# Performance work log

Measured on AMD Instinct MI355X. Metric: run time of the kernel, lower is better.

## Reference

```python
import jax, jax.numpy as jnp
import numpy as np

# dims
F, V, E, NIN, NOUT = 4, 4, 64, 1024, 1024
M = NIN + 2
# args constants
GMIN, GMAX, EPS, PGMIN = 0.01, 1.0, 0.1, 0.1
ETA2 = 0.25          # ACT[0].eta_fault[0,2]
ACT_T, NEG_T = 1.0, 1.0

# stand-in printed-electronics nonlinearities (ACT list and INV list)
_ACT = [lambda z: jax.nn.sigmoid(4.0 * (z - 0.5)), lambda z: jnp.tanh(z)]
_INV = [lambda a: 1.0 - a, lambda a: jax.nn.sigmoid(4.0 * (0.5 - a))]


def setup_inputs() -> dict:
    key = jax.random.key(0)
    ks = jax.random.split(key, 8)
    a = jax.random.uniform(ks[0], (F, V, E, NIN), jnp.float32)
    theta = jax.random.uniform(ks[1], (M, NOUT), jnp.float32) / 100.0 + GMIN
    theta = theta.at[-1, :].add(GMAX)
    theta = theta.at[-2, :].set(ETA2 / (1.0 - ETA2) * (theta[:-2, :].sum(0) + theta[-1, :]))
    coeff_act = jax.random.uniform(ks[2], (2, NOUT), jnp.float32, minval=-0.5, maxval=0.5)
    coeff_neg = jax.random.uniform(ks[3], (2, M), jnp.float32, minval=-0.5, maxval=0.5)
    noise_u = jax.random.uniform(ks[4], (F, V, M, NOUT), jnp.float32)
    gum = lambda k, s: -jnp.log(-jnp.log(jax.random.uniform(k, s, jnp.float32) + 1e-20) + 1e-20)
    gum_act = gum(ks[5], (2, NOUT))
    gum_neg = gum(ks[6], (2, M))
    fault_mask = jnp.ones((F, M, NOUT), jnp.float32)
    return dict(a=a, theta_=theta, coeff_act=coeff_act, coeff_neg=coeff_neg,
                noise_u=noise_u, gum_act=gum_act, gum_neg=gum_neg, fault_mask=fault_mask)


def _st_clip(x, lo, hi):
    sg = jax.lax.stop_gradient
    return x + sg(jnp.clip(x, lo, hi) - x)


def _gumbel_st(c, g, temp):
    # clamp, gumbel-softmax, hard argmax with straight-through estimator
    sg = jax.lax.stop_gradient
    cc = _st_clip(c, -1.0, 1.0)
    alpha = jax.nn.softmax((cc + g) / temp, axis=0)
    hard = jax.nn.one_hot(jnp.argmax(alpha, 0), c.shape[0], axis=0, dtype=alpha.dtype)
    return sg(hard) + alpha - sg(alpha)


def _forward(a, theta_, coeff_act, coeff_neg, noise_u, gum_act, gum_neg, fault_mask):
    sg = jax.lax.stop_gradient
    # theta property: clamp, zero small magnitudes (straight-through)
    tc = _st_clip(theta_, -GMAX, GMAX)
    tz = jnp.where(jnp.abs(tc) < GMIN, 0.0, tc)
    theta = sg(tz) + tc - sg(tc)
    # theta_noisy [F,V,M,N]: repeat + multiplicative uniform noise + fault mask
    tn = theta[None, None] * ((noise_u * 2.0 - 1.0) * EPS + 1.0) * fault_mask[:, None]
    at = jnp.abs(tn)
    W = at / (at.sum(axis=2, keepdims=True) + 1e-10)
    pos = (tn >= 0).astype(W.dtype)
    neg = 1.0 - pos
    # a_extend [F,V,E,M]: append bias-one and zero columns
    ones = jnp.ones(a.shape[:3] + (1,), a.dtype)
    ax = jnp.concatenate([a, ones, jnp.zeros_like(ones)], axis=-1)
    beta = _gumbel_st(coeff_neg, gum_neg, NEG_T)      # [2,M]
    an = beta[0] * _INV[0](ax) + beta[1] * _INV[1](ax)
    an = an.at[..., -1].set(0.0)
    z = (jnp.einsum('fvem,fvmn->fven', ax, W * pos)
         + jnp.einsum('fvem,fvmn->fven', an, W * neg))
    # MAC_power: vectorized expansion of sum_{f,v,m,n} g[m,n]*||sel - y||^2 over e
    gi = jnp.abs(tc)
    gt = gi * (PGMIN / gi.min(axis=0, keepdims=True))  # g_tilde [M,N]
    p = sg(pos)
    q = 1.0 - p
    AA = jnp.einsum('fvem,fvem->fvm', ax, ax)
    BB = jnp.einsum('fvem,fvem->fvm', an, an)
    AY = jnp.einsum('fvem,fven->fvmn', ax, z)
    BY = jnp.einsum('fvem,fven->fvmn', an, z)
    YY = jnp.einsum('fven,fven->fvn', z, z)
    power = (jnp.einsum('mn,fvmn,fvm->', gt, p, AA)
             + jnp.einsum('mn,fvmn,fvm->', gt, q, BB)
             - 2.0 * (jnp.einsum('mn,fvmn,fvmn->', gt, p, AY)
                      + jnp.einsum('mn,fvmn,fvmn->', gt, q, BY))
             + jnp.einsum('n,fvn->', gt.sum(0), YY)) / (E * V * F)
    # Gumbel-mixed activation
    alpha = _gumbel_st(coeff_act, gum_act, ACT_T)      # [2,N]
    a_new = alpha[0] * _ACT[0](z) + alpha[1] * _ACT[1](z)
    return a_new, power


def reference(a, theta_, coeff_act, coeff_neg, noise_u, gum_act, gum_neg, fault_mask):
    return _forward(a, theta_, coeff_act, coeff_neg, noise_u, gum_act, gum_neg, fault_mask)
```

## Files before the change

### kernel.cpp

```cpp
#include <hip/hip_runtime.h>

typedef float f32x4 __attribute__((ext_vector_type(4)));
typedef short bf16x8 __attribute__((ext_vector_type(8)));

#define NE 64
#define ND 1024
#define MM 1026

#define WS_GMINP 1050624
#define WS_GABSP 1083392
#define WS_AA    1642504
#define WS_BB    1658888
#define WS_TFG   1675272
#define WS_AXB   5877768
#define WS_ANB   6402056
#define POWER_IDX 1048576

__device__ __forceinline__ float frcp(float x) { return __builtin_amdgcn_rcpf(x); }
__device__ __forceinline__ unsigned f2b(float x) {
  unsigned u = __float_as_uint(x);
  u += 0x7FFF + ((u >> 16) & 1);
  return u >> 16;
}
__device__ __forceinline__ float b2f(unsigned b) { return __uint_as_float(b << 16); }
__device__ __forceinline__ float clamp1(float x) { return fminf(fmaxf(x, -1.f), 1.f); }

__global__ __launch_bounds__(256) void k_pre(
    const float* __restrict__ a, const float* __restrict__ theta_,
    const float* __restrict__ fault, const float* __restrict__ coeff_neg,
    const float* __restrict__ gum_neg, float* __restrict__ ws,
    float* __restrict__ out) {
  int bid = blockIdx.x, t = threadIdx.x;
  __shared__ float la[256][8];
  __shared__ float lb[256][8];
  __shared__ float beta_l[32];

  if (bid < 512) {
    int f = bid >> 7, chunk = bid & 127;
    int m0 = chunk * 8, m1 = (chunk == 127) ? MM : m0 + 8;
    unsigned* tfg = (unsigned*)(ws + WS_TFG) + (size_t)f * MM * ND;
    const float* fslab = fault + (size_t)f * MM * ND;
    int n4 = t * 4;
    for (int m = m0; m < m1; m++) {
      float4 tv = *(const float4*)(theta_ + m * ND + n4);
      float4 fl = *(const float4*)(fslab + (size_t)m * ND + n4);
      float c0 = clamp1(tv.x), c1 = clamp1(tv.y), c2 = clamp1(tv.z), c3 = clamp1(tv.w);
      float z0 = fabsf(c0), z1 = fabsf(c1), z2 = fabsf(c2), z3 = fabsf(c3);
      float w0 = (z0 < 0.01f ? 0.f : c0) * fl.x;
      float w1 = (z1 < 0.01f ? 0.f : c1) * fl.y;
      float w2 = (z2 < 0.01f ? 0.f : c2) * fl.z;
      float w3 = (z3 < 0.01f ? 0.f : c3) * fl.w;
      uint4 o;
      o.x = (f2b(z0) << 16) | f2b(w0);
      o.y = (f2b(z1) << 16) | f2b(w1);
      o.z = (f2b(z2) << 16) | f2b(w2);
      o.w = (f2b(z3) << 16) | f2b(w3);
      *(uint4*)(tfg + (size_t)m * ND + n4) = o;
    }
  } else if (bid < 1024) {
    int bb = bid - 512;
    int kc = bb & 31, fv = bb >> 5;
    if (t < 32) {
      int m = kc * 32 + t;
      float c0 = clamp1(coeff_neg[m]);
      float c1 = clamp1(coeff_neg[MM + m]);
      beta_l[t] = ((c1 + gum_neg[MM + m]) > (c0 + gum_neg[m])) ? 1.f : 0.f;
    }
    __syncthreads();
    int em = t >> 6, l = t & 63;
    int e = em * 16 + (l & 15);
    int g = (l >> 4) & 3;
    int kk = kc * 32 + g * 4;
    const float* ap = a + ((size_t)fv * NE + e) * 1024;
    float4 x0 = *(const float4*)(ap + kk);
    float4 x1 = *(const float4*)(ap + kk + 16);
    float xs[8] = {x0.x, x0.y, x0.z, x0.w, x1.x, x1.y, x1.z, x1.w};
    unsigned axp[8], anp[8];
#pragma unroll
    for (int j = 0; j < 8; j++) {
      int mloc = g * 4 + ((j < 4) ? j : 12 + j);
      float x = xs[j];
      float bs = beta_l[mloc];
      float an = (bs != 0.f) ? frcp(1.f + __expf(fmaf(4.f, x, -2.f))) : (1.f - x);
      axp[j] = f2b(x);
      anp[j] = f2b(an);
      la[t][j] = x * x;
      lb[t][j] = an * an;
    }
    uint4 ox = {axp[0] | (axp[1] << 16), axp[2] | (axp[3] << 16),
                axp[4] | (axp[5] << 16), axp[6] | (axp[7] << 16)};
    uint4 on = {anp[0] | (anp[1] << 16), anp[2] | (anp[3] << 16),
                anp[4] | (anp[5] << 16), anp[6] | (anp[7] << 16)};
    size_t bidx = ((size_t)(fv * 32 + kc) * 4 + em) * 64 + l;
    ((uint4*)(ws + WS_AXB))[bidx] = ox;
    ((uint4*)(ws + WS_ANB))[bidx] = on;
    __syncthreads();
    if (t < 32) {
      int g2 = (t >> 2) & 3, j2 = (t & 3) + 4 * (t >> 4);
      float sa = 0.f, sb = 0.f;
#pragma unroll
      for (int em2 = 0; em2 < 4; em2++)
#pragma unroll
        for (int i = 0; i < 16; i++) {
          sa += la[em2 * 64 + g2 * 16 + i][j2];
          sb += lb[em2 * 64 + g2 * 16 + i][j2];
        }
      ws[WS_AA + fv * 1024 + kc * 32 + t] = sa;
      ws[WS_BB + fv * 1024 + kc * 32 + t] = sb;
    }
  } else {
    int r = bid - 1024;
    int ng = r & 3, chunk = r >> 2;
    int n = ng * 256 + t;
    int m0 = chunk * 32, m1 = (chunk == 31) ? MM : m0 + 32;
    float mn = 1e30f, sm = 0.f;
    for (int m = m0; m < m1; m++) {
      float g = fabsf(clamp1(theta_[m * ND + n]));
      mn = fminf(mn, g);
      sm += g;
    }
    ws[WS_GMINP + chunk * ND + n] = mn;
    ws[WS_GABSP + chunk * ND + n] = sm;
    if (r == 0 && t == 0) out[POWER_IDX] = 0.f;
  }
}

union U8 { uint4 u; bf16x8 h; };

#define SLOAD(S, MC)                                                       \
  {                                                                        \
    _Pragma("unroll") for (int r = 0; r < 4; r++) {                        \
      size_t row = (size_t)((MC) + mb + r) * ND;                           \
      uA##S[r] = nslab[row + n0 + nin];                                    \
      uB##S[r] = nslab[row + n0 + 16 + nin];                               \
      tgA##S[r] = tslab[row + n0 + nin];                                   \
      tgB##S[r] = tslab[row + n0 + 16 + nin];                              \
    }                                                                      \
  }

#define AABBLOAD(MC)                                                       \
  {                                                                        \
    aa0 = *(const float4*)(AAp + (MC) + mb);                               \
    bb0 = *(const float4*)(BBp + (MC) + mb);                               \
  }

#define SWRITE(P, S)                                                       \
  {                                                                        \
    float aas[4] = {aa0.x, aa0.y, aa0.z, aa0.w};                           \
    float bbs[4] = {bb0.x, bb0.y, bb0.z, bb0.w};                           \
    unsigned wpu[2][4], wnu[2][4], gpu[2][4], gqu[2][4];                   \
    _Pragma("unroll") for (int h = 0; h < 2; h++) {                        \
      _Pragma("unroll") for (int r = 0; r < 4; r++) {                      \
        unsigned tg = h ? tgB##S[r] : tgA##S[r];                           \
        float u = h ? uB##S[r] : uA##S[r];                                 \
        unsigned neg = (tg >> 15) & 1;                                     \
        float aw = b2f(tg & 0x7FFF) * fmaf(u, 0.2f, 0.9f);                 \
        if (h) sacc1 += aw; else sacc0 += aw;                              \
        unsigned wb = f2b(aw);                                             \
        unsigned gb = tg >> 16;                                            \
        wpu[h][r] = neg ? 0u : wb;  wnu[h][r] = neg ? wb : 0u;             \
        gpu[h][r] = neg ? 0u : gb;  gqu[h][r] = neg ? gb : 0u;             \
        float tca = b2f(gb);                                               \
        float t1c = tca * (neg ? bbs[r] : aas[r]);                         \
        if (h) pacc1b += t1c; else pacc1a += t1c;                          \
      }                                                                    \
    }                                                                      \
    _Pragma("unroll") for (int pn = 0; pn < 4; pn++) {                     \
      uint2* pp = (uint2*)&panels[P][pn][0];                               \
      _Pragma("unroll") for (int h = 0; h < 2; h++) {                      \
        const unsigned* v = pn == 0 ? wpu[h] : pn == 1 ? wnu[h]            \
                             : pn == 2 ? gpu[h] : gqu[h];                  \
        int s0i = ((c_s * 2 + h) * 64 + (g0 & 3) * 16 + nin) * 2 + j0q;    \
        pp[s0i] = make_uint2(v[0] | (v[1] << 16), v[2] | (v[3] << 16));    \
      }                                                                    \
    }                                                                      \
  }

#define ALOAD(KS)                                                          \
  {                                                                        \
    _Pragma("unroll") for (int c = 0; c < 2; c++)                          \
      _Pragma("unroll") for (int mi = 0; mi < 2; mi++) {                   \
        size_t bi = ((size_t)(fv * 32 + (KS) * 2 + c) * 4 + eh * 2 + mi) * 64 + l; \
        axr[c][mi] = axbp[bi];                                             \
        anr[c][mi] = anbp[bi];                                             \
      }                                                                    \
  }

#define BMFMA(P)                                                           \
  {                                                                        \
    _Pragma("unroll") for (int c = 0; c < 2; c++) {                        \
      int bslot = (c * 2 + wn) * 64 + l;                                   \
      U8 bwp, bwn, bgp, bgq;                                               \
      bwp.u = panels[P][0][bslot]; bwn.u = panels[P][1][bslot];            \
      bgp.u = panels[P][2][bslot]; bgq.u = panels[P][3][bslot];            \
      _Pragma("unroll") for (int mi = 0; mi < 2; mi++) {                   \
        U8 ax, an; ax.u = axr[c][mi]; an.u = anr[c][mi];                   \
        accz[mi] = __builtin_amdgcn_mfma_f32_16x16x32_bf16(ax.h, bwp.h, accz[mi], 0, 0, 0); \
        accz[mi] = __builtin_amdgcn_mfma_f32_16x16x32_bf16(an.h, bwn.h, accz[mi], 0, 0, 0); \
        accg[mi] = __builtin_amdgcn_mfma_f32_16x16x32_bf16(ax.h, bgp.h, accg[mi], 0, 0, 0); \
        accg[mi] = __builtin_amdgcn_mfma_f32_16x16x32_bf16(an.h, bgq.h, accg[mi], 0, 0, 0); \
      }                                                                    \
    }                                                                      \
  }

#define BAR() __syncthreads()

__global__ __launch_bounds__(256) void k_main(
    const float* __restrict__ noise, const float* __restrict__ ws_c,
    const float* __restrict__ coeff_act, const float* __restrict__ gum_act,
    const float* __restrict__ coeff_neg, const float* __restrict__ gum_neg,
    float* __restrict__ out) {
  const int tid = threadIdx.x;
  const int w4 = tid >> 6, l = tid & 63;
  const int wn = w4 & 1;
  const int eh = w4 >> 1;
  const int fv = blockIdx.y, f = fv >> 2;
  const int n0 = blockIdx.x * 32;

  __shared__ uint4 panels[2][4][256];
  __shared__ float smin_l[32], gabs_l[32], s_l[32], gsum_l[32];

  if (tid < 32) {
    float mn = 1e30f;
#pragma unroll 8
    for (int c = 0; c < 32; c++) mn = fminf(mn, ws_c[WS_GMINP + c * ND + n0 + tid]);
    smin_l[tid] = mn;
  } else if (tid < 64) {
    int n = tid - 32;
    float s = 0.f;
#pragma unroll 8
    for (int c = 0; c < 32; c++) s += ws_c[WS_GABSP + c * ND + n0 + n];
    gabs_l[n] = s;
  }
  __syncthreads();
  if (tid < 32) {
    float s = 0.1f * frcp(smin_l[tid]);
    s_l[tid] = s;
    gsum_l[tid] = s * gabs_l[tid];
  }

  const int nin = tid & 15;
  const int mb = (tid >> 4) * 4;
  const int c_s = mb >> 5;
  const int g0 = (mb & 31) >> 2;
  const int j0q = (mb & 31) >> 4;
  const unsigned* tslab = (const unsigned*)(ws_c + WS_TFG) + (size_t)f * MM * ND;
  const float* nslab = noise + (size_t)fv * MM * ND;
  const float* AAp = ws_c + WS_AA + fv * 1024;
  const float* BBp = ws_c + WS_BB + fv * 1024;
  const uint4* axbp = (const uint4*)(ws_c + WS_AXB);
  const uint4* anbp = (const uint4*)(ws_c + WS_ANB);

  float pacc = 0.f, pacc1a = 0.f, pacc1b = 0.f, sacc0 = 0.f, sacc1 = 0.f;
  float uA0[4], uB0[4], uA1[4], uB1[4];
  unsigned tgA0[4], tgB0[4], tgA1[4], tgB1[4];
  float4 aa0, bb0;
  uint4 axr[2][2], anr[2][2];
  f32x4 accz[2] = {};
  f32x4 accg[2] = {};

  AABBLOAD(0);
  SLOAD(0, 0);
  SWRITE(0, 0);
  SLOAD(1, 64);
  BAR();

  for (int ks2 = 0; ks2 < 16; ks2 += 2) {
    ALOAD(ks2);
    AABBLOAD((ks2 + 1) * 64);
    if (ks2 < 14) SLOAD(0, (ks2 + 2) * 64);
    SWRITE(1, 1);
    BMFMA(0);
    BAR();
    ALOAD(ks2 + 1);
    if (ks2 < 14) {
      AABBLOAD((ks2 + 2) * 64);
      SLOAD(1, (ks2 + 3) * 64);
      SWRITE(0, 0);
    }
    BMFMA(1);
    BAR();
  }

  float* lds_f = (float*)&panels[0][0][0];
  lds_f[(tid >> 4) * 32 + nin] = sacc0;
  lds_f[(tid >> 4) * 32 + 16 + nin] = sacc1;
  __syncthreads();

  const int n_loc = wn * 16 + (l & 15);
  const int n_e = n0 + n_loc;
  float S = 0.f;
#pragma unroll
  for (int mg = 0; mg < 16; mg++) S += lds_f[mg * 32 + n_loc];

  const float s_ne = s_l[n_loc];
  unsigned tg24 = tslab[(size_t)1024 * ND + n_e];
  unsigned tg25 = tslab[(size_t)1025 * ND + n_e];
  float u24 = nslab[(size_t)1024 * ND + n_e];
  float u25 = nslab[(size_t)1025 * ND + n_e];
  float w24 = b2f(tg24 & 0x7FFF) * fmaf(u24, 0.2f, 0.9f);
  float w25 = b2f(tg25 & 0x7FFF) * fmaf(u25, 0.2f, 0.9f);
  S += w24 + w25;
  const float invS = frcp(S + 1e-10f);

  float cn0 = clamp1(coeff_neg[1024]), cn1 = clamp1(coeff_neg[MM + 1024]);
  const float anb = ((cn1 + gum_neg[MM + 1024]) > (cn0 + gum_neg[1024]))
                        ? frcp(1.f + __expf(2.f)) : 0.f;
  float ca0 = clamp1(coeff_act[n_e]), ca1 = clamp1(coeff_act[ND + n_e]);
  const float alv = ((ca1 + gum_act[ND + n_e]) > (ca0 + gum_act[n_e])) ? 1.f : 0.f;

  unsigned neg24 = (tg24 >> 15) & 1;
  float sel24 = neg24 ? anb : 1.f;
  float ztail = w24 * invS * sel24;
  float gt24 = b2f(tg24 >> 16) * s_ne;
  if (l < 16 && eh == 0) pacc += 64.f * gt24 * sel24 * sel24;

  const float gsn = gsum_l[n_loc];
  float zsum = 0.f;
#pragma unroll
  for (int mi = 0; mi < 2; mi++) {
#pragma unroll
    for (int r = 0; r < 4; r++) {
      float z = accz[mi][r] * invS + ztail;
      zsum += z;
      pacc += gsn * z * z - 2.f * z * (accg[mi][r] * s_ne);
      float s0v = frcp(1.f + __expf(fmaf(-4.f, z, 2.f)));
      float t1v = 1.f - 2.f * frcp(__expf(2.f * z) + 1.f);
      int e = (eh * 2 + mi) * 16 + ((l >> 4) & 3) * 4 + r;
      out[((size_t)(fv * NE + e)) * ND + n_e] = (alv != 0.f) ? t1v : s0v;
    }
  }
  pacc -= 2.f * zsum * (gt24 * sel24);
  pacc += s_l[nin] * pacc1a + s_l[16 + nin] * pacc1b;

  float* red = lds_f + 1024;
  red[tid] = pacc;
  __syncthreads();
  for (int s = 128; s > 0; s >>= 1) {
    if (tid < s) red[tid] += red[tid + s];
    __syncthreads();
  }
  if (tid == 0) atomicAdd(out + POWER_IDX, red[0] * (1.f / 1024.f));
}

extern "C" void kernel_launch(void* const* d_in, const int* in_sizes, int n_in,
                              void* d_out, int out_size, void* d_ws, size_t ws_size,
                              hipStream_t stream) {
  const float* a = (const float*)d_in[0];
  const float* theta_ = (const float*)d_in[1];
  const float* coeff_act = (const float*)d_in[2];
  const float* coeff_neg = (const float*)d_in[3];
  const float* noise_u = (const float*)d_in[4];
  const float* gum_act = (const float*)d_in[5];
  const float* gum_neg = (const float*)d_in[6];
  const float* fault = (const float*)d_in[7];
  float* out = (float*)d_out;
  float* ws = (float*)d_ws;

  k_pre<<<1152, 256, 0, stream>>>(a, theta_, fault, coeff_neg, gum_neg, ws, out);
  k_main<<<dim3(32, 16), 256, 0, stream>>>(noise_u, ws, coeff_act, gum_act,
                                           coeff_neg, gum_neg, out);
}
```

Measured before the change: 174.3 us.

## Fold per-column theta min/sum reduction into main kernel's streaming loop

Removes the separate k_pre branch that reduced |theta| per column into partial min/sum buffers, and instead computes column min and sum inside k_main from the bf16 |theta| values it already streams, reducing them through LDS at the end. The theta-packing work in k_pre is split into more, smaller blocks, with the two tail rows handled by four extra blocks. Noise loads are marked nontemporal. The intent is to drop a pass over theta and the prologue reductions in k_main, at the cost of using bf16-rounded |theta| for the min/sum and extra LDS traffic.

After: 163.2 us. 1.07x faster.

```diff
diff --git a/kernel.cpp b/kernel.cpp
--- a/kernel.cpp
+++ b/kernel.cpp
@@ -7,8 +7,6 @@
 #define ND 1024
 #define MM 1026
 
-#define WS_GMINP 1050624
-#define WS_GABSP 1083392
 #define WS_AA    1642504
 #define WS_BB    1658888
 #define WS_TFG   1675272
@@ -35,13 +33,15 @@
   __shared__ float lb[256][8];
   __shared__ float beta_l[32];
 
-  if (bid < 512) {
-    int f = bid >> 7, chunk = bid & 127;
-    int m0 = chunk * 8, m1 = (chunk == 127) ? MM : m0 + 8;
+  if (bid < 1024) {
+    int f = bid >> 8, chunk = bid & 255;
+    int m0 = chunk * 4;
     unsigned* tfg = (unsigned*)(ws + WS_TFG) + (size_t)f * MM * ND;
     const float* fslab = fault + (size_t)f * MM * ND;
     int n4 = t * 4;
-    for (int m = m0; m < m1; m++) {
+#pragma unroll
+    for (int r = 0; r < 4; r++) {
+      int m = m0 + r;
       float4 tv = *(const float4*)(theta_ + m * ND + n4);
       float4 fl = *(const float4*)(fslab + (size_t)m * ND + n4);
       float c0 = clamp1(tv.x), c1 = clamp1(tv.y), c2 = clamp1(tv.z), c3 = clamp1(tv.w);
@@ -57,8 +57,9 @@
       o.w = (f2b(z3) << 16) | f2b(w3);
       *(uint4*)(tfg + (size_t)m * ND + n4) = o;
     }
-  } else if (bid < 1024) {
-    int bb = bid - 512;
+    if (bid == 0 && t == 0) out[POWER_IDX] = 0.f;
+  } else if (bid < 1536) {
+    int bb = bid - 1024;
     int kc = bb & 31, fv = bb >> 5;
     if (t < 32) {
       int m = kc * 32 + t;
@@ -109,19 +110,28 @@
       ws[WS_BB + fv * 1024 + kc * 32 + t] = sb;
     }
   } else {
-    int r = bid - 1024;
-    int ng = r & 3, chunk = r >> 2;
-    int n = ng * 256 + t;
-    int m0 = chunk * 32, m1 = (chunk == 31) ? MM : m0 + 32;
-    float mn = 1e30f, sm = 0.f;
-    for (int m = m0; m < m1; m++) {
-      float g = fabsf(clamp1(theta_[m * ND + n]));
-      mn = fminf(mn, g);
-      sm += g;
-    }
-    ws[WS_GMINP + chunk * ND + n] = mn;
-    ws[WS_GABSP + chunk * ND + n] = sm;
-    if (r == 0 && t == 0) out[POWER_IDX] = 0.f;
+    int f = bid - 1536;
+    unsigned* tfg = (unsigned*)(ws + WS_TFG) + (size_t)f * MM * ND;
+    const float* fslab = fault + (size_t)f * MM * ND;
+    int n4 = t * 4;
+#pragma unroll
+    for (int r = 0; r < 2; r++) {
+      int m = 1024 + r;
+      float4 tv = *(const float4*)(theta_ + m * ND + n4);
+      float4 fl = *(const float4*)(fslab + (size_t)m * ND + n4);
+      float c0 = clamp1(tv.x), c1 = clamp1(tv.y), c2 = clamp1(tv.z), c3 = clamp1(tv.w);
+      float z0 = fabsf(c0), z1 = fabsf(c1), z2 = fabsf(c2), z3 = fabsf(c3);
+      float w0 = (z0 < 0.01f ? 0.f : c0) * fl.x;
+      float w1 = (z1 < 0.01f ? 0.f : c1) * fl.y;
+      float w2 = (z2 < 0.01f ? 0.f : c2) * fl.z;
+      float w3 = (z3 < 0.01f ? 0.f : c3) * fl.w;
+      uint4 o;
+      o.x = (f2b(z0) << 16) | f2b(w0);
+      o.y = (f2b(z1) << 16) | f2b(w1);
+      o.z = (f2b(z2) << 16) | f2b(w2);
+      o.w = (f2b(z3) << 16) | f2b(w3);
+      *(uint4*)(tfg + (size_t)m * ND + n4) = o;
+    }
   }
 }
 
@@ -131,8 +141,8 @@
   {                                                                        \
     _Pragma("unroll") for (int r = 0; r < 4; r++) {                        \
       size_t row = (size_t)((MC) + mb + r) * ND;                           \
-      uA##S[r] = nslab[row + n0 + nin];                                    \
-      uB##S[r] = nslab[row + n0 + 16 + nin];                               \
+      uA##S[r] = __builtin_nontemporal_load(nslab + row + n0 + nin);       \
+      uB##S[r] = __builtin_nontemporal_load(nslab + row + n0 + 16 + nin);  \
       tgA##S[r] = tslab[row + n0 + nin];                                   \
       tgB##S[r] = tslab[row + n0 + 16 + nin];                              \
     }                                                                      \
@@ -162,7 +172,8 @@
         gpu[h][r] = neg ? 0u : gb;  gqu[h][r] = neg ? gb : 0u;             \
         float tca = b2f(gb);                                               \
         float t1c = tca * (neg ? bbs[r] : aas[r]);                         \
-        if (h) pacc1b += t1c; else pacc1a += t1c;                          \
+        if (h) { pacc1b += t1c; mnacc1 = fminf(mnacc1, tca); gsacc1 += tca; } \
+        else   { pacc1a += t1c; mnacc0 = fminf(mnacc0, tca); gsacc0 += tca; } \
       }                                                                    \
     }                                                                      \
     _Pragma("unroll") for (int pn = 0; pn < 4; pn++) {                     \
@@ -218,26 +229,6 @@
   const int n0 = blockIdx.x * 32;
 
   __shared__ uint4 panels[2][4][256];
-  __shared__ float smin_l[32], gabs_l[32], s_l[32], gsum_l[32];
-
-  if (tid < 32) {
-    float mn = 1e30f;
-#pragma unroll 8
-    for (int c = 0; c < 32; c++) mn = fminf(mn, ws_c[WS_GMINP + c * ND + n0 + tid]);
-    smin_l[tid] = mn;
-  } else if (tid < 64) {
-    int n = tid - 32;
-    float s = 0.f;
-#pragma unroll 8
-    for (int c = 0; c < 32; c++) s += ws_c[WS_GABSP + c * ND + n0 + n];
-    gabs_l[n] = s;
-  }
-  __syncthreads();
-  if (tid < 32) {
-    float s = 0.1f * frcp(smin_l[tid]);
-    s_l[tid] = s;
-    gsum_l[tid] = s * gabs_l[tid];
-  }
 
   const int nin = tid & 15;
   const int mb = (tid >> 4) * 4;
@@ -252,6 +243,7 @@
   const uint4* anbp = (const uint4*)(ws_c + WS_ANB);
 
   float pacc = 0.f, pacc1a = 0.f, pacc1b = 0.f, sacc0 = 0.f, sacc1 = 0.f;
+  float mnacc0 = 1e30f, mnacc1 = 1e30f, gsacc0 = 0.f, gsacc1 = 0.f;
   float uA0[4], uB0[4], uA1[4], uB1[4];
   unsigned tgA0[4], tgB0[4], tgA1[4], tgB1[4];
   float4 aa0, bb0;
@@ -283,17 +275,23 @@
   }
 
   float* lds_f = (float*)&panels[0][0][0];
-  lds_f[(tid >> 4) * 32 + nin] = sacc0;
-  lds_f[(tid >> 4) * 32 + 16 + nin] = sacc1;
+  const int gi_ = (tid >> 4) * 32;
+  lds_f[gi_ + nin] = sacc0;           lds_f[gi_ + 16 + nin] = sacc1;
+  lds_f[512 + gi_ + nin] = mnacc0;    lds_f[512 + gi_ + 16 + nin] = mnacc1;
+  lds_f[1024 + gi_ + nin] = gsacc0;   lds_f[1024 + gi_ + 16 + nin] = gsacc1;
+  lds_f[1536 + gi_ + nin] = pacc1a;   lds_f[1536 + gi_ + 16 + nin] = pacc1b;
   __syncthreads();
 
   const int n_loc = wn * 16 + (l & 15);
   const int n_e = n0 + n_loc;
-  float S = 0.f;
-#pragma unroll
-  for (int mg = 0; mg < 16; mg++) S += lds_f[mg * 32 + n_loc];
-
-  const float s_ne = s_l[n_loc];
+  float S = 0.f, MN = 1e30f, GS = 0.f;
+#pragma unroll
+  for (int mg = 0; mg < 16; mg++) {
+    S += lds_f[mg * 32 + n_loc];
+    MN = fminf(MN, lds_f[512 + mg * 32 + n_loc]);
+    GS += lds_f[1024 + mg * 32 + n_loc];
+  }
+
   unsigned tg24 = tslab[(size_t)1024 * ND + n_e];
   unsigned tg25 = tslab[(size_t)1025 * ND + n_e];
   float u24 = nslab[(size_t)1024 * ND + n_e];
@@ -303,6 +301,12 @@
   S += w24 + w25;
   const float invS = frcp(S + 1e-10f);
 
+  float tc24a = b2f(tg24 >> 16), tc25a = b2f(tg25 >> 16);
+  MN = fminf(MN, fminf(tc24a, tc25a));
+  GS += tc24a + tc25a;
+  const float s_ne = 0.1f * frcp(MN);
+  const float gsn = s_ne * GS;
+
   float cn0 = clamp1(coeff_neg[1024]), cn1 = clamp1(coeff_neg[MM + 1024]);
   const float anb = ((cn1 + gum_neg[MM + 1024]) > (cn0 + gum_neg[1024]))
                         ? frcp(1.f + __expf(2.f)) : 0.f;
@@ -312,10 +316,14 @@
   unsigned neg24 = (tg24 >> 15) & 1;
   float sel24 = neg24 ? anb : 1.f;
   float ztail = w24 * invS * sel24;
-  float gt24 = b2f(tg24 >> 16) * s_ne;
-  if (l < 16 && eh == 0) pacc += 64.f * gt24 * sel24 * sel24;
-
-  const float gsn = gsum_l[n_loc];
+  float gt24 = tc24a * s_ne;
+  if (eh == 0 && ((l >> 4) & 3) == 0) {
+    float P1 = 0.f;
+#pragma unroll
+    for (int mg = 0; mg < 16; mg++) P1 += lds_f[1536 + mg * 32 + n_loc];
+    pacc += s_ne * P1 + 64.f * gt24 * sel24 * sel24;
+  }
+
   float zsum = 0.f;
 #pragma unroll
   for (int mi = 0; mi < 2; mi++) {
@@ -331,9 +339,8 @@
     }
   }
   pacc -= 2.f * zsum * (gt24 * sel24);
-  pacc += s_l[nin] * pacc1a + s_l[16 + nin] * pacc1b;
-
-  float* red = lds_f + 1024;
+
+  float* red = lds_f + 2048;
   red[tid] = pacc;
   __syncthreads();
   for (int s = 128; s > 0; s >>= 1) {
@@ -357,7 +364,7 @@
   float* out = (float*)d_out;
   float* ws = (float*)d_ws;
 
-  k_pre<<<1152, 256, 0, stream>>>(a, theta_, fault, coeff_neg, gum_neg, ws, out);
+  k_pre<<<1540, 256, 0, stream>>>(a, theta_, fault, coeff_neg, gum_neg, ws, out);
   k_main<<<dim3(32, 16), 256, 0, stream>>>(noise_u, ws, coeff_act, gum_act,
                                            coeff_neg, gum_neg, out);
 }
```
